# Performance work log

Hardware: AMD Instinct MI355X
Metric: run time of the kernel (lower is better)

## Reference

```python
import jax, jax.numpy as jnp
import numpy as np

BETA = 0.5  # exp-sum normalization exponent (not a true softmax)


def setup_inputs() -> dict:
    key = jax.random.key(0)
    ks = jax.random.split(key, 12)
    b, h = 1024, 200
    item_num, region_num, user_num = 50000, 1000, 10000
    d, hid = 128, 128  # embed_size == hidden_size (required by the bmm reshape)
    std = 0.01
    return {
        "history": jax.random.randint(ks[0], (1, b, h), 0, item_num),
        "target": jax.random.randint(ks[1], (1, b), 0, item_num),
        "history_region": jax.random.randint(ks[2], (1, b, h), 0, region_num),
        "target_region": jax.random.randint(ks[3], (1, b), 0, region_num),
        "history_visit_rate": jax.random.uniform(ks[4], (1, h), dtype=jnp.float32),
        "dist_mat": jax.random.uniform(ks[5], (b, h), dtype=jnp.float32),
        "uid": 7,
        "embed_target": std * jax.random.normal(ks[6], (item_num, d // 2), dtype=jnp.float32),
        "embed_region": std * jax.random.normal(ks[7], (region_num, d // 2), dtype=jnp.float32),
        "embed_dist": std * jax.random.normal(ks[8], (user_num, region_num), dtype=jnp.float32),
        "Wq": jax.random.normal(ks[9], (hid, d), dtype=jnp.float32) * (1.0 / np.sqrt(d)),
        "Wk": jax.random.normal(ks[10], (hid, d), dtype=jnp.float32) * (1.0 / np.sqrt(d)),
        "Wv": jax.random.normal(ks[11], (d, d), dtype=jnp.float32) * (1.0 / np.sqrt(d)),
    }


def reference(history, target, history_region, target_region, history_visit_rate,
              dist_mat, uid, embed_target, embed_region, embed_dist, Wq, Wk, Wv):
    h_idx = history[0]            # [b, h]
    tgt = target[0]               # [b]
    hr = history_region[0]        # [b, h]
    tr = target_region[0]         # [b]
    hv = history_visit_rate[0]    # [h]
    b, hlen = h_idx.shape

    # embedding gathers + concat (target half | region half)
    hist_emb = jnp.concatenate([embed_target[h_idx], embed_region[hr]], axis=-1)  # [b,h,d]
    tgt_emb = jnp.concatenate([embed_target[tgt], embed_region[tr]], axis=-1)     # [b,d]
    hd = embed_dist[uid][hr]      # [b, h]
    td = embed_dist[uid][tr]      # [b]
    d = tgt_emb.shape[1]

    # QKV projections (torch Linear: y = x @ W.T)
    q = tgt_emb @ Wq.T            # [b, d]  (hidden == d)
    k = hist_emb @ Wk.T           # [b, h, d]
    v = hist_emb @ Wv.T           # [b, h, d]

    # faithful to original: key reshaped (NOT transposed) to [b, d, h]
    k_r = k.reshape(b, d, hlen)
    scores = jnp.einsum('bd,bdh->bh', q, k_r) / jnp.sqrt(jnp.float32(d))  # [b,h]

    # exp / beta-normalized attention with equality mask
    mask = (h_idx != tgt[:, None]).astype(scores.dtype)
    exp_A = jnp.exp(scores) * mask                          # [b,h]
    exp_sum = jnp.sum(exp_A, axis=-1) ** BETA               # [b]
    attn = exp_A / exp_sum[:, None]                         # [b,h]

    # geo weights: td @ hd is a vector-matrix product -> [h], broadcast over b
    geo = jnp.exp(-1.0 / (jax.nn.relu(td @ hd) + 1.0) * dist_mat)  # [b,h]

    result1 = v * (attn + geo)[..., None]                   # [b,h,d]
    result2 = hist_emb * jnp.broadcast_to(hv, (b, hlen))[..., None]
    result = result1 + result2                              # [b,h,d]

    pred = jnp.einsum('bhd,bd->b', result, tgt_emb)         # bmm + sum over h
    return jax.nn.sigmoid(pred)
```

## Files before the change

### kernel.cpp

```cpp
#include <hip/hip_runtime.h>

typedef unsigned short USH;
typedef unsigned int   UIN;

static constexpr int Bn = 1024;
static constexpr int Hn = 200;
static constexpr int Dn = 128;
static constexpr int Dh = 64;
static constexpr int NITEM = 50000;
static constexpr int NREG  = 1000;
static constexpr int MT = 64;
static constexpr int AB_A_BLOCKS = (NITEM + MT - 1) / MT;
static constexpr int AB_B_BLOCKS = (NREG  + MT - 1) / MT;
static constexpr int WTS = 132;
static constexpr int ETS = 69;

__device__ __forceinline__ float bf2f(USH u) {
  return __uint_as_float(((UIN)u) << 16);
}
__device__ __forceinline__ float2 pb2f2(UIN p) {
  float2 r;
  r.x = __uint_as_float(p << 16);
  r.y = __uint_as_float(p & 0xffff0000u);
  return r;
}
__device__ __forceinline__ USH f2b(float f) {
  UIN x = __float_as_uint(f);
  return (USH)((x + 0x7fffu + ((x >> 16) & 1u)) >> 16);
}
__device__ __forceinline__ UIN addpk(UIN u, UIN v) {
  float2 a = pb2f2(u), b = pb2f2(v);
  return (UIN)f2b(a.x + b.x) | ((UIN)f2b(a.y + b.y) << 16);
}

__global__ __launch_bounds__(256) void g_kernel(
    const int* __restrict__ hregion, const int* __restrict__ tregion,
    const float* __restrict__ embed_dist, const int* __restrict__ uid,
    float* __restrict__ g) {
  int c = threadIdx.x;
  const float* row = embed_dist + (size_t)uid[0] * NREG;
  float acc = 0.f;
  int ibase = blockIdx.x * 16;
  for (int ii = 0; ii < 16; ii++) {
    int i = ibase + ii;
    float td = row[tregion[i]];
    if (c < Hn) acc += td * row[hregion[(size_t)i * Hn + c]];
  }
  if (c < Hn) atomicAdd(&g[c], acc);
}

__global__ __launch_bounds__(256, 2) void ab_kernel(
    const float* __restrict__ Et, const float* __restrict__ Er,
    const float* __restrict__ Wk, USH* __restrict__ A, USH* __restrict__ Bt,
    USH* __restrict__ Ebr, USH* __restrict__ Err, int emit_raw) {
  __shared__ float wt[64 * WTS];
  __shared__ float et[MT * ETS];
  int blk = blockIdx.x, tid = threadIdx.x;
  const float* E; USH* Out; USH* OutR; int nmax, base, koff;
  if (blk < AB_A_BLOCKS) { E = Et; Out = A;  OutR = Ebr; nmax = NITEM; base = blk * MT; koff = 0; }
  else { E = Er; Out = Bt; OutR = Err; nmax = NREG; base = (blk - AB_A_BLOCKS) * MT; koff = 64; }

#pragma unroll
  for (int p = 0; p < 8; p++) {
    int idx = p * 256 + tid;
    int row = idx >> 4, c4 = idx & 15;
    float4 w = *reinterpret_cast<const float4*>(Wk + (size_t)row * Dn + koff + c4 * 4);
    wt[(c4 * 4 + 0) * WTS + row] = w.x;
    wt[(c4 * 4 + 1) * WTS + row] = w.y;
    wt[(c4 * 4 + 2) * WTS + row] = w.z;
    wt[(c4 * 4 + 3) * WTS + row] = w.w;
  }
#pragma unroll
  for (int p = 0; p < 4; p++) {
    int idx = p * 256 + tid;
    int m = idx >> 4, c4 = idx & 15;
    int gi = base + m;
    float4 e = make_float4(0.f, 0.f, 0.f, 0.f);
    if (gi < nmax) e = *reinterpret_cast<const float4*>(E + (size_t)gi * Dh + c4 * 4);
    et[m * ETS + c4 * 4 + 0] = e.x;
    et[m * ETS + c4 * 4 + 1] = e.y;
    et[m * ETS + c4 * 4 + 2] = e.z;
    et[m * ETS + c4 * 4 + 3] = e.w;
  }
  __syncthreads();

  if (emit_raw) {
#pragma unroll
    for (int q = 0; q < 8; q++) {
      int idx = q * 256 + tid;
      int m = idx >> 5, kp = idx & 31;
      int gi = base + m;
      if (gi < nmax) {
        UIN pk = (UIN)f2b(et[m * ETS + 2 * kp]) | ((UIN)f2b(et[m * ETS + 2 * kp + 1]) << 16);
        *reinterpret_cast<UIN*>(OutR + (size_t)gi * Dh + 2 * kp) = pk;
      }
    }
  }

  int jt = tid & 15, it = tid >> 4;
  const float* wb = wt + jt * 8;
  const float* eb = et + (it * 4) * ETS;
  float c[4][8];
#pragma unroll
  for (int ii = 0; ii < 4; ii++)
#pragma unroll
    for (int jj = 0; jj < 8; jj++) c[ii][jj] = 0.f;

#pragma unroll 2
  for (int k = 0; k < 64; k++) {
    float4 w0 = *reinterpret_cast<const float4*>(wb + (size_t)k * WTS);
    float4 w1 = *reinterpret_cast<const float4*>(wb + (size_t)k * WTS + 4);
    float e0 = eb[k], e1 = eb[ETS + k], e2 = eb[2 * ETS + k], e3 = eb[3 * ETS + k];
    c[0][0] += e0 * w0.x; c[0][1] += e0 * w0.y; c[0][2] += e0 * w0.z; c[0][3] += e0 * w0.w;
    c[0][4] += e0 * w1.x; c[0][5] += e0 * w1.y; c[0][6] += e0 * w1.z; c[0][7] += e0 * w1.w;
    c[1][0] += e1 * w0.x; c[1][1] += e1 * w0.y; c[1][2] += e1 * w0.z; c[1][3] += e1 * w0.w;
    c[1][4] += e1 * w1.x; c[1][5] += e1 * w1.y; c[1][6] += e1 * w1.z; c[1][7] += e1 * w1.w;
    c[2][0] += e2 * w0.x; c[2][1] += e2 * w0.y; c[2][2] += e2 * w0.z; c[2][3] += e2 * w0.w;
    c[2][4] += e2 * w1.x; c[2][5] += e2 * w1.y; c[2][6] += e2 * w1.z; c[2][7] += e2 * w1.w;
    c[3][0] += e3 * w0.x; c[3][1] += e3 * w0.y; c[3][2] += e3 * w0.z; c[3][3] += e3 * w0.w;
    c[3][4] += e3 * w1.x; c[3][5] += e3 * w1.y; c[3][6] += e3 * w1.z; c[3][7] += e3 * w1.w;
  }

#pragma unroll
  for (int ii = 0; ii < 4; ii++) {
    int item = base + it * 4 + ii;
    if (item < nmax) {
      uint4 pk;
      pk.x = (UIN)f2b(c[ii][0]) | ((UIN)f2b(c[ii][1]) << 16);
      pk.y = (UIN)f2b(c[ii][2]) | ((UIN)f2b(c[ii][3]) << 16);
      pk.z = (UIN)f2b(c[ii][4]) | ((UIN)f2b(c[ii][5]) << 16);
      pk.w = (UIN)f2b(c[ii][6]) | ((UIN)f2b(c[ii][7]) << 16);
      *reinterpret_cast<uint4*>(Out + (size_t)item * Dn + jt * 8) = pk;
    }
  }
}

__global__ __launch_bounds__(256, 3) void main_kernel(
    const int* __restrict__ history, const int* __restrict__ target,
    const int* __restrict__ hregion, const int* __restrict__ tregion,
    const float* __restrict__ hv, const float* __restrict__ dist_mat,
    const float* __restrict__ Et, const float* __restrict__ Er,
    const float* __restrict__ Wq, const float* __restrict__ Wv,
    const float* __restrict__ g, const USH* __restrict__ A,
    const USH* __restrict__ Bt, const USH* __restrict__ Ebr,
    const USH* __restrict__ Err, int use_raw, float* __restrict__ out) {
  __shared__ USH kvs[Hn * Dn];
  __shared__ float tgtE[128], qv[128], uv[128];
  __shared__ float red[8];
  int i = blockIdx.x, tid = threadIdx.x, lane = tid & 63, wave = tid >> 6;
  int tgt_i = target[i], tr_i = tregion[i];
  const int* hrow = history + (size_t)i * Hn;
  const int* rrow = hregion + (size_t)i * Hn;

  if (tid < 64)       tgtE[tid] = Et[(size_t)tgt_i * Dh + tid];
  else if (tid < 128) tgtE[tid] = Er[(size_t)tr_i * Dh + (tid - 64)];

  {
    int rlane = tid & 15, rgrp = tid >> 4;
#pragma unroll
    for (int p = 0; p < 13; p++) {
      int t = p * 16 + rgrp;
      if (t < Hn) {
        int ia = hrow[t], ib = rrow[t];
        uint4 av = *reinterpret_cast<const uint4*>(A  + (size_t)ia * Dn + rlane * 8);
        uint4 bv = *reinterpret_cast<const uint4*>(Bt + (size_t)ib * Dn + rlane * 8);
        uint4 pk;
        pk.x = addpk(av.x, bv.x); pk.y = addpk(av.y, bv.y);
        pk.z = addpk(av.z, bv.z); pk.w = addpk(av.w, bv.w);
        *reinterpret_cast<uint4*>(&kvs[t * Dn + rlane * 8]) = pk;
      }
    }
  }
  __syncthreads();

  if (tid < 128) {
    int j = tid; float acc = 0.f;
    const float4* wp = reinterpret_cast<const float4*>(Wq + (size_t)j * Dn);
#pragma unroll
    for (int q4 = 0; q4 < 32; q4++) {
      float4 w = wp[q4];
      const float* tv = &tgtE[q4 * 4];
      acc += w.x * tv[0] + w.y * tv[1] + w.z * tv[2] + w.w * tv[3];
    }
    qv[j] = acc * 0.088388347648318447f;
  } else {
    int d = tid - 128;
    float a0 = 0.f, a1 = 0.f, a2 = 0.f, a3 = 0.f;
#pragma unroll 8
    for (int j = 0; j < 128; j += 4) {
      a0 += Wv[(size_t)(j + 0) * Dn + d] * tgtE[j + 0];
      a1 += Wv[(size_t)(j + 1) * Dn + d] * tgtE[j + 1];
      a2 += Wv[(size_t)(j + 2) * Dn + d] * tgtE[j + 2];
      a3 += Wv[(size_t)(j + 3) * Dn + d] * tgtE[j + 3];
    }
    uv[d] = (a0 + a1) + (a2 + a3);
  }
  __syncthreads();

  float ea = 0.f, sc1 = 0.f, sc2 = 0.f;
  if (tid < Hn) {
    int c = tid;
    float acc = 0.f;
    const USH* kp = &kvs[c];
#pragma unroll 16
    for (int a = 0; a < 128; a++) acc += qv[a] * bf2f(kp[a * 200]);
    int ia2 = hrow[tid], ib2 = rrow[tid];
    float p1 = 0.f, p2 = 0.f;
    if (use_raw) {
      const uint4* epu = reinterpret_cast<const uint4*>(Ebr + (size_t)ia2 * Dh);
      const uint4* rpu = reinterpret_cast<const uint4*>(Err + (size_t)ib2 * Dh);
#pragma unroll
      for (int k8 = 0; k8 < 8; k8++) {
        uint4 e = epu[k8], r = rpu[k8];
        float2 e0 = pb2f2(e.x), e1 = pb2f2(e.y), e2 = pb2f2(e.z), e3 = pb2f2(e.w);
        float2 r0 = pb2f2(r.x), r1 = pb2f2(r.y), r2 = pb2f2(r.z), r3 = pb2f2(r.w);
        const float* u0 = &uv[k8 * 8];       const float* t0 = &tgtE[k8 * 8];
        const float* u1 = &uv[64 + k8 * 8];  const float* t1 = &tgtE[64 + k8 * 8];
        p1 += e0.x * u0[0] + e0.y * u0[1] + e1.x * u0[2] + e1.y * u0[3]
            + e2.x * u0[4] + e2.y * u0[5] + e3.x * u0[6] + e3.y * u0[7]
            + r0.x * u1[0] + r0.y * u1[1] + r1.x * u1[2] + r1.y * u1[3]
            + r2.x * u1[4] + r2.y * u1[5] + r3.x * u1[6] + r3.y * u1[7];
        p2 += e0.x * t0[0] + e0.y * t0[1] + e1.x * t0[2] + e1.y * t0[3]
            + e2.x * t0[4] + e2.y * t0[5] + e3.x * t0[6] + e3.y * t0[7]
            + r0.x * t1[0] + r0.y * t1[1] + r1.x * t1[2] + r1.y * t1[3]
            + r2.x * t1[4] + r2.y * t1[5] + r3.x * t1[6] + r3.y * t1[7];
      }
    } else {
      const float4* ep = reinterpret_cast<const float4*>(Et + (size_t)ia2 * Dh);
      const float4* rp = reinterpret_cast<const float4*>(Er + (size_t)ib2 * Dh);
#pragma unroll
      for (int k4 = 0; k4 < 16; k4++) {
        float4 e = ep[k4], r = rp[k4];
        const float* u0 = &uv[k4 * 4];        const float* t0 = &tgtE[k4 * 4];
        const float* u1 = &uv[64 + k4 * 4];   const float* t1 = &tgtE[64 + k4 * 4];
        p1 += e.x * u0[0] + e.y * u0[1] + e.z * u0[2] + e.w * u0[3]
            + r.x * u1[0] + r.y * u1[1] + r.z * u1[2] + r.w * u1[3];
        p2 += e.x * t0[0] + e.y * t0[1] + e.z * t0[2] + e.w * t0[3]
            + r.x * t1[0] + r.y * t1[1] + r.z * t1[2] + r.w * t1[3];
      }
    }
    sc1 = p1; sc2 = p2;
    ea = (ia2 != tgt_i) ? __expf(acc) : 0.f;
  }

  float wsum = ea;
  for (int off = 32; off > 0; off >>= 1) wsum += __shfl_down(wsum, off, 64);
  if (lane == 0) red[wave] = wsum;
  __syncthreads();
  float esum = red[0] + red[1] + red[2] + red[3];
  float inv = esum > 0.f ? 1.f / sqrtf(esum) : 0.f;

  float part = 0.f;
  if (tid < Hn) {
    float attn = ea * inv;
    float gc = g[tid]; gc = gc > 0.f ? gc : 0.f;
    float dm = dist_mat[(size_t)i * Hn + tid];
    float geo = __expf(-dm / (gc + 1.f));
    part = (attn + geo) * sc1 + hv[tid] * sc2;
  }
  __syncthreads();
  for (int off = 32; off > 0; off >>= 1) part += __shfl_down(part, off, 64);
  if (lane == 0) red[wave] = part;
  __syncthreads();
  if (tid == 0) {
    float pred = red[0] + red[1] + red[2] + red[3];
    out[i] = 1.f / (1.f + __expf(-pred));
  }
}

extern "C" void kernel_launch(void* const* d_in, const int* in_sizes, int n_in,
                              void* d_out, int out_size, void* d_ws, size_t ws_size,
                              hipStream_t stream) {
  const int*   history = (const int*)d_in[0];
  const int*   target  = (const int*)d_in[1];
  const int*   hregion = (const int*)d_in[2];
  const int*   tregion = (const int*)d_in[3];
  const float* hv      = (const float*)d_in[4];
  const float* dist    = (const float*)d_in[5];
  const int*   uid     = (const int*)d_in[6];
  const float* Et      = (const float*)d_in[7];
  const float* Er      = (const float*)d_in[8];
  const float* Edist   = (const float*)d_in[9];
  const float* Wq      = (const float*)d_in[10];
  const float* Wk      = (const float*)d_in[11];
  const float* Wv      = (const float*)d_in[12];

  float* g = (float*)d_ws;
  USH* A   = (USH*)((char*)d_ws + 1024);
  USH* Bt  = A + (size_t)NITEM * Dn;
  USH* Ebr = Bt + (size_t)NREG * Dn;
  USH* Err = Ebr + (size_t)NITEM * Dh;
  size_t need_raw = 1024 + 2 * ((size_t)NITEM * Dn + (size_t)NREG * Dn +
                                (size_t)NITEM * Dh + (size_t)NREG * Dh);
  int use_raw = (ws_size >= need_raw) ? 1 : 0;
  float* out = (float*)d_out;

  hipMemsetAsync(g, 0, Hn * sizeof(float), stream);
  g_kernel<<<Bn / 16, 256, 0, stream>>>(hregion, tregion, Edist, uid, g);
  ab_kernel<<<AB_A_BLOCKS + AB_B_BLOCKS, 256, 0, stream>>>(Et, Er, Wk, A, Bt,
                                                           Ebr, Err, use_raw);
  main_kernel<<<Bn, 256, 0, stream>>>(history, target, hregion, tregion, hv, dist,
                                      Et, Er, Wq, Wv, g, A, Bt, Ebr, Err, use_raw,
                                      out);
}
```

Before: 176.1 us.

## Stage key rows in two halves to halve LDS and raise occupancy

The per-block shared buffer of gathered key/value rows is cut from 200 to 100 rows. The kernel now gathers the first half, computes the first 64 terms of each score dot product, then gathers the second half into the same buffer and finishes the scores. Because of the faithful reshape, score element a reads flat offset a*200+tid, so the first 64 terms fall in rows 0-99 and the rest in rows 100-199, which makes the split consistent. Less LDS per block lets more blocks fit on each CU, and launch bounds move from 3 to 5 blocks. The cost is an extra barrier and a second serialized gather phase per block, plus tighter register limits that could cause spills.

Measured after the change: 179.2 us. About the same (+1.8%).

```diff
diff --git a/kernel.cpp b/kernel.cpp
--- a/kernel.cpp
+++ b/kernel.cpp
@@ -14,6 +14,7 @@
 static constexpr int AB_B_BLOCKS = (NREG  + MT - 1) / MT;
 static constexpr int WTS = 132;
 static constexpr int ETS = 69;
+static constexpr int KROWS = 100;
 
 __device__ __forceinline__ float bf2f(USH u) {
   return __uint_as_float(((UIN)u) << 16);
@@ -135,7 +136,7 @@
   }
 }
 
-__global__ __launch_bounds__(256, 3) void main_kernel(
+__global__ __launch_bounds__(256, 5) void main_kernel(
     const int* __restrict__ history, const int* __restrict__ target,
     const int* __restrict__ hregion, const int* __restrict__ tregion,
     const float* __restrict__ hv, const float* __restrict__ dist_mat,
@@ -144,7 +145,7 @@
     const float* __restrict__ g, const USH* __restrict__ A,
     const USH* __restrict__ Bt, const USH* __restrict__ Ebr,
     const USH* __restrict__ Err, int use_raw, float* __restrict__ out) {
-  __shared__ USH kvs[Hn * Dn];
+  __shared__ USH kvs[KROWS * Dn];
   __shared__ float tgtE[128], qv[128], uv[128];
   __shared__ float red[8];
   int i = blockIdx.x, tid = threadIdx.x, lane = tid & 63, wave = tid >> 6;
@@ -155,20 +156,18 @@
   if (tid < 64)       tgtE[tid] = Et[(size_t)tgt_i * Dh + tid];
   else if (tid < 128) tgtE[tid] = Er[(size_t)tr_i * Dh + (tid - 64)];
 
-  {
-    int rlane = tid & 15, rgrp = tid >> 4;
-#pragma unroll
-    for (int p = 0; p < 13; p++) {
-      int t = p * 16 + rgrp;
-      if (t < Hn) {
-        int ia = hrow[t], ib = rrow[t];
-        uint4 av = *reinterpret_cast<const uint4*>(A  + (size_t)ia * Dn + rlane * 8);
-        uint4 bv = *reinterpret_cast<const uint4*>(Bt + (size_t)ib * Dn + rlane * 8);
-        uint4 pk;
-        pk.x = addpk(av.x, bv.x); pk.y = addpk(av.y, bv.y);
-        pk.z = addpk(av.z, bv.z); pk.w = addpk(av.w, bv.w);
-        *reinterpret_cast<uint4*>(&kvs[t * Dn + rlane * 8]) = pk;
-      }
+  int rlane = tid & 15, rgrp = tid >> 4;
+#pragma unroll
+  for (int p = 0; p < 7; p++) {
+    int t = p * 16 + rgrp;
+    if (t < KROWS) {
+      int ia = hrow[t], ib = rrow[t];
+      uint4 av = *reinterpret_cast<const uint4*>(A  + (size_t)ia * Dn + rlane * 8);
+      uint4 bv = *reinterpret_cast<const uint4*>(Bt + (size_t)ib * Dn + rlane * 8);
+      uint4 pk;
+      pk.x = addpk(av.x, bv.x); pk.y = addpk(av.y, bv.y);
+      pk.z = addpk(av.z, bv.z); pk.w = addpk(av.w, bv.w);
+      *reinterpret_cast<uint4*>(&kvs[t * Dn + rlane * 8]) = pk;
     }
   }
   __syncthreads();
@@ -197,13 +196,8 @@
   }
   __syncthreads();
 
-  float ea = 0.f, sc1 = 0.f, sc2 = 0.f;
+  float ea = 0.f, sc1 = 0.f, sc2 = 0.f, acc = 0.f;
   if (tid < Hn) {
-    int c = tid;
-    float acc = 0.f;
-    const USH* kp = &kvs[c];
-#pragma unroll 16
-    for (int a = 0; a < 128; a++) acc += qv[a] * bf2f(kp[a * 200]);
     int ia2 = hrow[tid], ib2 = rrow[tid];
     float p1 = 0.f, p2 = 0.f;
     if (use_raw) {
@@ -240,7 +234,32 @@
       }
     }
     sc1 = p1; sc2 = p2;
-    ea = (ia2 != tgt_i) ? __expf(acc) : 0.f;
+    const USH* kp = &kvs[tid];
+#pragma unroll 16
+    for (int a = 0; a < 64; a++) acc += qv[a] * bf2f(kp[a * 200]);
+  }
+  __syncthreads();
+
+#pragma unroll
+  for (int p = 0; p < 7; p++) {
+    int t = KROWS + p * 16 + rgrp;
+    if (t < Hn) {
+      int ia = hrow[t], ib = rrow[t];
+      uint4 av = *reinterpret_cast<const uint4*>(A  + (size_t)ia * Dn + rlane * 8);
+      uint4 bv = *reinterpret_cast<const uint4*>(Bt + (size_t)ib * Dn + rlane * 8);
+      uint4 pk;
+      pk.x = addpk(av.x, bv.x); pk.y = addpk(av.y, bv.y);
+      pk.z = addpk(av.z, bv.z); pk.w = addpk(av.w, bv.w);
+      *reinterpret_cast<uint4*>(&kvs[(t - KROWS) * Dn + rlane * 8]) = pk;
+    }
+  }
+  __syncthreads();
+
+  if (tid < Hn) {
+    const USH* kp = &kvs[tid];
+#pragma unroll 16
+    for (int a = 0; a < 64; a++) acc += qv[64 + a] * bf2f(kp[a * 200]);
+    ea = (hrow[tid] != tgt_i) ? __expf(acc) : 0.f;
   }
 
   float wsum = ea;
```

## Split score computation into a 4-way per-row kernel and a separate epilogue kernel

Applied to the files above, without the earlier changes.

The monolithic main kernel is split in two. A new score kernel runs four blocks per batch row, and each block gathers only 50 history rows of keys (the 32 reshaped d-slices) into a much smaller shared buffer, computing partial attention scores. A separate epilogue kernel sums the four partials and does the value, geo and visit-rate projection plus the sigmoid. This is meant to cut the large shared-memory footprint that limited occupancy and to spread the key gather across more blocks. In exchange it adds a kernel launch and a global-memory round trip for the partial scores, and the partial-score buffer is placed in the workspace even when the raw-buffer size check fails.

Result: no change. 172.7 us (-1.9%).

```diff
diff --git a/kernel.cpp b/kernel.cpp
--- a/kernel.cpp
+++ b/kernel.cpp
@@ -14,6 +14,7 @@
 static constexpr int AB_B_BLOCKS = (NREG  + MT - 1) / MT;
 static constexpr int WTS = 132;
 static constexpr int ETS = 69;
+static constexpr int CR = 50;
 
 __device__ __forceinline__ float bf2f(USH u) {
   return __uint_as_float(((UIN)u) << 16);
@@ -135,18 +136,75 @@
   }
 }
 
-__global__ __launch_bounds__(256, 3) void main_kernel(
+__global__ __launch_bounds__(256, 4) void sc_kernel(
+    const int* __restrict__ history, const int* __restrict__ target,
+    const int* __restrict__ hregion, const int* __restrict__ tregion,
+    const float* __restrict__ Et, const float* __restrict__ Er,
+    const float* __restrict__ Wq, const USH* __restrict__ A,
+    const USH* __restrict__ Bt, float* __restrict__ psc) {
+  __shared__ USH kvs[CR * Dn];
+  __shared__ float tgtE[128], qp[128], qv[32];
+  int b = blockIdx.x, i = b >> 2, h = b & 3;
+  int tid = threadIdx.x;
+  const int* hrow = history + (size_t)i * Hn + CR * h;
+  const int* rrow = hregion + (size_t)i * Hn + CR * h;
+
+  if (tid < 64)       tgtE[tid] = Et[(size_t)target[i] * Dh + tid];
+  else if (tid < 128) tgtE[tid] = Er[(size_t)tregion[i] * Dh + (tid - 64)];
+
+  int rlane = tid & 15, rgrp = tid >> 4;
+#pragma unroll
+  for (int p = 0; p < 4; p++) {
+    int t = p * 16 + rgrp;
+    if (t < CR) {
+      int ia = hrow[t], ib = rrow[t];
+      uint4 av = *reinterpret_cast<const uint4*>(A  + (size_t)ia * Dn + rlane * 8);
+      uint4 bv = *reinterpret_cast<const uint4*>(Bt + (size_t)ib * Dn + rlane * 8);
+      uint4 pk;
+      pk.x = addpk(av.x, bv.x); pk.y = addpk(av.y, bv.y);
+      pk.z = addpk(av.z, bv.z); pk.w = addpk(av.w, bv.w);
+      *reinterpret_cast<uint4*>(&kvs[t * Dn + rlane * 8]) = pk;
+    }
+  }
+  __syncthreads();
+
+  if (tid < 128) {
+    int ql = tid >> 2, quarter = tid & 3;
+    int a = 32 * h + ql;
+    const float4* wp = reinterpret_cast<const float4*>(Wq + (size_t)a * Dn + quarter * 32);
+    float acc = 0.f;
+#pragma unroll
+    for (int k4 = 0; k4 < 8; k4++) {
+      float4 w = wp[k4];
+      const float* tv = &tgtE[quarter * 32 + k4 * 4];
+      acc += w.x * tv[0] + w.y * tv[1] + w.z * tv[2] + w.w * tv[3];
+    }
+    qp[tid] = acc;
+  }
+  __syncthreads();
+  if (tid < 32)
+    qv[tid] = (qp[4 * tid] + qp[4 * tid + 1] + qp[4 * tid + 2] + qp[4 * tid + 3])
+              * 0.088388347648318447f;
+  __syncthreads();
+
+  if (tid < Hn) {
+    float acc = 0.f;
+    const USH* kp = &kvs[tid];
+#pragma unroll
+    for (int a = 0; a < 32; a++) acc += qv[a] * bf2f(kp[a * 200]);
+    psc[((size_t)i * 4 + h) * Hn + tid] = acc;
+  }
+}
+
+__global__ __launch_bounds__(256, 4) void ep_kernel(
     const int* __restrict__ history, const int* __restrict__ target,
     const int* __restrict__ hregion, const int* __restrict__ tregion,
     const float* __restrict__ hv, const float* __restrict__ dist_mat,
     const float* __restrict__ Et, const float* __restrict__ Er,
-    const float* __restrict__ Wq, const float* __restrict__ Wv,
-    const float* __restrict__ g, const USH* __restrict__ A,
-    const USH* __restrict__ Bt, const USH* __restrict__ Ebr,
-    const USH* __restrict__ Err, int use_raw, float* __restrict__ out) {
-  __shared__ USH kvs[Hn * Dn];
-  __shared__ float tgtE[128], qv[128], uv[128];
-  __shared__ float red[8];
+    const float* __restrict__ Wv, const float* __restrict__ g,
+    const USH* __restrict__ Ebr, const USH* __restrict__ Err,
+    const float* __restrict__ psc, int use_raw, float* __restrict__ out) {
+  __shared__ float tgtE[128], uv[128], red[8];
   int i = blockIdx.x, tid = threadIdx.x, lane = tid & 63, wave = tid >> 6;
   int tgt_i = target[i], tr_i = tregion[i];
   const int* hrow = history + (size_t)i * Hn;
@@ -154,36 +212,9 @@
 
   if (tid < 64)       tgtE[tid] = Et[(size_t)tgt_i * Dh + tid];
   else if (tid < 128) tgtE[tid] = Er[(size_t)tr_i * Dh + (tid - 64)];
-
-  {
-    int rlane = tid & 15, rgrp = tid >> 4;
-#pragma unroll
-    for (int p = 0; p < 13; p++) {
-      int t = p * 16 + rgrp;
-      if (t < Hn) {
-        int ia = hrow[t], ib = rrow[t];
-        uint4 av = *reinterpret_cast<const uint4*>(A  + (size_t)ia * Dn + rlane * 8);
-        uint4 bv = *reinterpret_cast<const uint4*>(Bt + (size_t)ib * Dn + rlane * 8);
-        uint4 pk;
-        pk.x = addpk(av.x, bv.x); pk.y = addpk(av.y, bv.y);
-        pk.z = addpk(av.z, bv.z); pk.w = addpk(av.w, bv.w);
-        *reinterpret_cast<uint4*>(&kvs[t * Dn + rlane * 8]) = pk;
-      }
-    }
-  }
-  __syncthreads();
-
-  if (tid < 128) {
-    int j = tid; float acc = 0.f;
-    const float4* wp = reinterpret_cast<const float4*>(Wq + (size_t)j * Dn);
-#pragma unroll
-    for (int q4 = 0; q4 < 32; q4++) {
-      float4 w = wp[q4];
-      const float* tv = &tgtE[q4 * 4];
-      acc += w.x * tv[0] + w.y * tv[1] + w.z * tv[2] + w.w * tv[3];
-    }
-    qv[j] = acc * 0.088388347648318447f;
-  } else {
+  __syncthreads();
+
+  if (tid >= 128) {
     int d = tid - 128;
     float a0 = 0.f, a1 = 0.f, a2 = 0.f, a3 = 0.f;
 #pragma unroll 8
@@ -199,11 +230,8 @@
 
   float ea = 0.f, sc1 = 0.f, sc2 = 0.f;
   if (tid < Hn) {
-    int c = tid;
-    float acc = 0.f;
-    const USH* kp = &kvs[c];
-#pragma unroll 16
-    for (int a = 0; a < 128; a++) acc += qv[a] * bf2f(kp[a * 200]);
+    const float* pp = psc + (size_t)i * 4 * Hn + tid;
+    float s = (pp[0] + pp[Hn]) + (pp[2 * Hn] + pp[3 * Hn]);
     int ia2 = hrow[tid], ib2 = rrow[tid];
     float p1 = 0.f, p2 = 0.f;
     if (use_raw) {
@@ -240,7 +268,7 @@
       }
     }
     sc1 = p1; sc2 = p2;
-    ea = (ia2 != tgt_i) ? __expf(acc) : 0.f;
+    ea = (ia2 != tgt_i) ? __expf(s) : 0.f;
   }
 
   float wsum = ea;
@@ -290,8 +318,10 @@
   USH* Bt  = A + (size_t)NITEM * Dn;
   USH* Ebr = Bt + (size_t)NREG * Dn;
   USH* Err = Ebr + (size_t)NITEM * Dh;
+  float* psc = (float*)(Err + (size_t)NREG * Dh);
   size_t need_raw = 1024 + 2 * ((size_t)NITEM * Dn + (size_t)NREG * Dn +
-                                (size_t)NITEM * Dh + (size_t)NREG * Dh);
+                                (size_t)NITEM * Dh + (size_t)NREG * Dh) +
+                    4 * (size_t)Bn * 4 * Hn;
   int use_raw = (ws_size >= need_raw) ? 1 : 0;
   float* out = (float*)d_out;
 
@@ -299,7 +329,8 @@
   g_kernel<<<Bn / 16, 256, 0, stream>>>(hregion, tregion, Edist, uid, g);
   ab_kernel<<<AB_A_BLOCKS + AB_B_BLOCKS, 256, 0, stream>>>(Et, Er, Wk, A, Bt,
                                                            Ebr, Err, use_raw);
-  main_kernel<<<Bn, 256, 0, stream>>>(history, target, hregion, tregion, hv, dist,
-                                      Et, Er, Wq, Wv, g, A, Bt, Ebr, Err, use_raw,
-                                      out);
-}
+  sc_kernel<<<Bn * 4, 256, 0, stream>>>(history, target, hregion, tregion,
+                                        Et, Er, Wq, A, Bt, psc);
+  ep_kernel<<<Bn, 256, 0, stream>>>(history, target, hregion, tregion, hv, dist,
+                                    Et, Er, Wv, g, Ebr, Err, psc, use_raw, out);
+}
```
